# Kernel optimization log

Measured on AMD Instinct MI355X. Metric: run time of the kernel, lower is better.

The kernel has to match this reference:

```python
import jax, jax.numpy as jnp
import numpy as np

B, T, H, DK = 16, 1024, 8, 64  # BN, seq_len, n_heads, d_model/n_heads


def setup_inputs() -> dict:
    key = jax.random.key(0)
    kq, kk, kv = jax.random.split(key, 3)
    queries = jax.random.normal(kq, (B, T, H, DK), dtype=jnp.float32)
    keys = jax.random.normal(kk, (B, T, H, DK), dtype=jnp.float32)
    values = jax.random.normal(kv, (B, T, H, DK), dtype=jnp.float32)
    attention_mask = jnp.zeros((B, H, T, T), dtype=bool)  # mask_flag=False -> unused
    return {"queries": queries, "keys": keys, "values": values,
            "attention_mask": attention_mask}


def reference(queries, keys, values, attention_mask):
    # queries/keys/values: [B, T, H, d]; mask_flag=False so attention_mask unused.
    d_k = queries.shape[-1]
    scale = 1.0 / np.sqrt(d_k).astype(np.float32)
    # scores[b,h,t,s] = sum_e q[b,t,h,e] * k[b,s,h,e]
    scores = jnp.einsum('bthe,bshe->bhts', queries, keys)
    A = jax.nn.softmax(scale * scores, axis=-1)  # dropout=identity (eval)
    V = jnp.einsum('bhts,bshd->bthd', A, values)
    return V
```

## Files before the change

kernel.cpp:

```cpp
#include <hip/hip_runtime.h>
#include <hip/hip_bf16.h>
#include <stdint.h>

typedef __bf16 bf16_t;
typedef bf16_t bf16x8 __attribute__((ext_vector_type(8)));
typedef bf16_t bf16x4 __attribute__((ext_vector_type(4)));
typedef float  f32x4  __attribute__((ext_vector_type(4)));
typedef float  f32x16 __attribute__((ext_vector_type(16)));

constexpr int Bsz = 16, Tsz = 1024, Hn = 8, Dk = 64;
constexpr int QB  = 512;
constexpr int KVB = 64;
constexpr int NIT = Tsz / KVB;
constexpr int STRIDE_T = Hn * Dk;
constexpr float QSCALE = 0.125f * 1.44269504f;

__global__ __launch_bounds__(1024, 4)
void fattn(const float* __restrict__ Q, const float* __restrict__ K,
           const float* __restrict__ V, float* __restrict__ O)
{
    const int orig = blockIdx.x;
    const int wg   = (orig & 7) * 32 + (orig >> 3);
    const int qt   = wg & 1;
    const int bh   = wg >> 1;
    const int h    = bh & (Hn - 1);
    const int b    = bh >> 3;

    const int tid  = threadIdx.x;
    const int warp = tid >> 6;
    const int lane = tid & 63;
    const int l31  = lane & 31;
    const int hi   = lane >> 5;

    __shared__ alignas(16) bf16_t Kl[2][KVB * Dk];
    __shared__ alignas(16) bf16_t Vl[2][Dk * KVB];

    const size_t base = (size_t)b * (Tsz * Hn * Dk) + (size_t)h * Dk;
    const float* Qb = Q + base;
    const float* Kb = K + base;
    const float* Vb = V + base;
    float*       Ob = O + base;

    bf16x8 qf[4];
    {
        const float* qs = Qb + (size_t)(qt * QB + warp * 32 + l31) * STRIDE_T + hi * 8;
        #pragma unroll
        for (int ks = 0; ks < 4; ++ks) {
            f32x4 lo = *reinterpret_cast<const f32x4*>(qs + ks * 16);
            f32x4 hh = *reinterpret_cast<const f32x4*>(qs + ks * 16 + 4);
            bf16x8 f;
            #pragma unroll
            for (int j = 0; j < 4; ++j) {
                f[j]     = (bf16_t)(lo[j] * QSCALE);
                f[4 + j] = (bf16_t)(hh[j] * QSCALE);
            }
            qf[ks] = f;
        }
    }

    const int kr  = tid >> 4;
    const int ke0 = (tid & 15) * 4;
    const float* kg = Kb + (size_t)kr * STRIDE_T + ke0;
    const uint32_t kidx = (uint32_t)(kr * Dk + ke0) ^ (uint32_t)((kr & 7) << 3);

    const int vd   = tid & 63;
    const int pos0 = (tid >> 6) * 4;
    const int vs0  = (pos0 & ~12) | ((pos0 & 4) << 1) | ((pos0 & 8) >> 1);
    const float* vgp = Vb + (size_t)vs0 * STRIDE_T + vd;
    const uint32_t vidx = (uint32_t)(vd * KVB + pos0) ^ (uint32_t)((vd & 7) << 3);

    const uint32_t swz = (uint32_t)((l31 & 7) << 3);

    f32x16 o0, o1;
    #pragma unroll
    for (int r = 0; r < 16; ++r) { o0[r] = 0.f; o1[r] = 0.f; }
    float l_acc = 0.f;

    f32x4 kra;
    float vv[4];
    kra = *reinterpret_cast<const f32x4*>(kg);
    #pragma unroll
    for (int j = 0; j < 4; ++j) vv[j] = vgp[(size_t)j * STRIDE_T];
    {
        bf16x4 kw;
        #pragma unroll
        for (int j = 0; j < 4; ++j) kw[j] = (bf16_t)kra[j];
        *reinterpret_cast<bf16x4*>(&Kl[0][kidx]) = kw;
        bf16x4 vw;
        #pragma unroll
        for (int j = 0; j < 4; ++j) vw[j] = (bf16_t)vv[j];
        *reinterpret_cast<bf16x4*>(&Vl[0][vidx]) = vw;
    }
    __syncthreads();

    for (int t = 0; t < NIT; ++t) {
        const int cur = t & 1;

        if (t + 1 < NIT) {
            kg  += (size_t)KVB * STRIDE_T;
            vgp += (size_t)KVB * STRIDE_T;
            kra = *reinterpret_cast<const f32x4*>(kg);
            #pragma unroll
            for (int j = 0; j < 4; ++j) vv[j] = vgp[(size_t)j * STRIDE_T];
        }


        f32x16 acc0, acc1;
        #pragma unroll
        for (int r = 0; r < 16; ++r) { acc0[r] = 0.f; acc1[r] = 0.f; }
        #pragma unroll
        for (int ks = 0; ks < 4; ++ks) {
            const uint32_t i0 = ((uint32_t)((l31) * Dk + ks * 16 + hi * 8)) ^ swz;
            bf16x8 af0 = *reinterpret_cast<const bf16x8*>(&Kl[cur][i0]);
            acc0 = __builtin_amdgcn_mfma_f32_32x32x16_bf16(af0, qf[ks], acc0, 0, 0, 0);
        }
        #pragma unroll
        for (int ks = 0; ks < 4; ++ks) {
            const uint32_t i1 = ((uint32_t)((32 + l31) * Dk + ks * 16 + hi * 8)) ^ swz;
            bf16x8 af1 = *reinterpret_cast<const bf16x8*>(&Kl[cur][i1]);
            acc1 = __builtin_amdgcn_mfma_f32_32x32x16_bf16(af1, qf[ks], acc1, 0, 0, 0);
        }

        bf16x8 pa00, pa01;
        {
            float p[16];
            #pragma unroll
            for (int r = 0; r < 16; ++r) p[r] = __builtin_exp2f(acc0[r]);
            l_acc += (((p[0]+p[1])+(p[2]+p[3]))+((p[4]+p[5])+(p[6]+p[7])))
                   + (((p[8]+p[9])+(p[10]+p[11]))+((p[12]+p[13])+(p[14]+p[15])));
            #pragma unroll
            for (int j = 0; j < 8; ++j) { pa00[j] = (bf16_t)p[j]; pa01[j] = (bf16_t)p[8+j]; }
        }

        #pragma unroll
        for (int ks2 = 0; ks2 < 2; ++ks2) {
            bf16x8 pa = ks2 ? pa01 : pa00;
            const uint32_t colb = (uint32_t)(ks2 * 16 + hi * 8);
            const uint32_t i0 = ((uint32_t)(l31 * KVB) + colb) ^ swz;
            bf16x8 vf0 = *reinterpret_cast<const bf16x8*>(&Vl[cur][i0]);
            o0 = __builtin_amdgcn_mfma_f32_32x32x16_bf16(vf0, pa, o0, 0, 0, 0);
            const uint32_t i1 = ((uint32_t)((32 + l31) * KVB) + colb) ^ swz;
            bf16x8 vf1 = *reinterpret_cast<const bf16x8*>(&Vl[cur][i1]);
            o1 = __builtin_amdgcn_mfma_f32_32x32x16_bf16(vf1, pa, o1, 0, 0, 0);
        }

        bf16x8 pa10, pa11;
        {
            float p[16];
            #pragma unroll
            for (int r = 0; r < 16; ++r) p[r] = __builtin_exp2f(acc1[r]);
            l_acc += (((p[0]+p[1])+(p[2]+p[3]))+((p[4]+p[5])+(p[6]+p[7])))
                   + (((p[8]+p[9])+(p[10]+p[11]))+((p[12]+p[13])+(p[14]+p[15])));
            #pragma unroll
            for (int j = 0; j < 8; ++j) { pa10[j] = (bf16_t)p[j]; pa11[j] = (bf16_t)p[8+j]; }
        }

        #pragma unroll
        for (int ks2 = 0; ks2 < 2; ++ks2) {
            bf16x8 pa = ks2 ? pa11 : pa10;
            const uint32_t colb = (uint32_t)(32 + ks2 * 16 + hi * 8);
            const uint32_t i0 = ((uint32_t)(l31 * KVB) + colb) ^ swz;
            bf16x8 vf0 = *reinterpret_cast<const bf16x8*>(&Vl[cur][i0]);
            o0 = __builtin_amdgcn_mfma_f32_32x32x16_bf16(vf0, pa, o0, 0, 0, 0);
            const uint32_t i1 = ((uint32_t)((32 + l31) * KVB) + colb) ^ swz;
            bf16x8 vf1 = *reinterpret_cast<const bf16x8*>(&Vl[cur][i1]);
            o1 = __builtin_amdgcn_mfma_f32_32x32x16_bf16(vf1, pa, o1, 0, 0, 0);
        }

        if (t + 1 < NIT) {
            bf16x4 kw;
            #pragma unroll
            for (int j = 0; j < 4; ++j) kw[j] = (bf16_t)kra[j];
            *reinterpret_cast<bf16x4*>(&Kl[cur ^ 1][kidx]) = kw;
            bf16x4 vw;
            #pragma unroll
            for (int j = 0; j < 4; ++j) vw[j] = (bf16_t)vv[j];
            *reinterpret_cast<bf16x4*>(&Vl[cur ^ 1][vidx]) = vw;
        }
        __syncthreads();
    }

    float l_tot = l_acc + __shfl_xor(l_acc, 32, 64);
    const float inv = 1.0f / l_tot;
    float* ob = Ob + (size_t)(qt * QB + warp * 32 + l31) * STRIDE_T;
    #pragma unroll
    for (int r = 0; r < 16; ++r) {
        const int d = (r & 3) + 8 * (r >> 2) + 4 * hi;
        ob[d]      = o0[r] * inv;
        ob[d + 32] = o1[r] * inv;
    }
}

extern "C" void kernel_launch(void* const* d_in, const int* in_sizes, int n_in,
                              void* d_out, int out_size, void* d_ws, size_t ws_size,
                              hipStream_t stream) {
    const float* Q = (const float*)d_in[0];
    const float* K = (const float*)d_in[1];
    const float* V = (const float*)d_in[2];
    float* O = (float*)d_out;

    const int nblocks = Bsz * Hn * (Tsz / QB);
    fattn<<<nblocks, 1024, 0, stream>>>(Q, K, V, O);
}
```

Before: 60.36 us.

## Halve query block to 256 rows with 512-thread blocks and 8-wide staging

```diff
diff --git a/kernel.cpp b/kernel.cpp
--- a/kernel.cpp
+++ b/kernel.cpp
@@ -4,25 +4,24 @@
 
 typedef __bf16 bf16_t;
 typedef bf16_t bf16x8 __attribute__((ext_vector_type(8)));
-typedef bf16_t bf16x4 __attribute__((ext_vector_type(4)));
 typedef float  f32x4  __attribute__((ext_vector_type(4)));
 typedef float  f32x16 __attribute__((ext_vector_type(16)));
 
 constexpr int Bsz = 16, Tsz = 1024, Hn = 8, Dk = 64;
-constexpr int QB  = 512;
+constexpr int QB  = 256;
 constexpr int KVB = 64;
 constexpr int NIT = Tsz / KVB;
 constexpr int STRIDE_T = Hn * Dk;
 constexpr float QSCALE = 0.125f * 1.44269504f;
 
-__global__ __launch_bounds__(1024, 4)
+__global__ __launch_bounds__(512, 4)
 void fattn(const float* __restrict__ Q, const float* __restrict__ K,
            const float* __restrict__ V, float* __restrict__ O)
 {
     const int orig = blockIdx.x;
-    const int wg   = (orig & 7) * 32 + (orig >> 3);
-    const int qt   = wg & 1;
-    const int bh   = wg >> 1;
+    const int wg   = (orig & 7) * 64 + (orig >> 3);
+    const int qt   = wg & 3;
+    const int bh   = wg >> 2;
     const int h    = bh & (Hn - 1);
     const int b    = bh >> 3;
 
@@ -58,14 +57,14 @@
         }
     }
 
-    const int kr  = tid >> 4;
-    const int ke0 = (tid & 15) * 4;
+    const int kr  = tid >> 3;
+    const int ke0 = (tid & 7) * 8;
     const float* kg = Kb + (size_t)kr * STRIDE_T + ke0;
     const uint32_t kidx = (uint32_t)(kr * Dk + ke0) ^ (uint32_t)((kr & 7) << 3);
 
     const int vd   = tid & 63;
-    const int pos0 = (tid >> 6) * 4;
-    const int vs0  = (pos0 & ~12) | ((pos0 & 4) << 1) | ((pos0 & 8) >> 1);
+    const int pos0 = (tid >> 6) * 8;
+    const int vs0  = (pos0 & ~8) | ((pos0 & 8) >> 1);
     const float* vgp = Vb + (size_t)vs0 * STRIDE_T + vd;
     const uint32_t vidx = (uint32_t)(vd * KVB + pos0) ^ (uint32_t)((vd & 7) << 3);
 
@@ -76,20 +75,24 @@
     for (int r = 0; r < 16; ++r) { o0[r] = 0.f; o1[r] = 0.f; }
     float l_acc = 0.f;
 
-    f32x4 kra;
-    float vv[4];
+    f32x4 kra, krb;
+    float vv[8];
     kra = *reinterpret_cast<const f32x4*>(kg);
+    krb = *reinterpret_cast<const f32x4*>(kg + 4);
     #pragma unroll
-    for (int j = 0; j < 4; ++j) vv[j] = vgp[(size_t)j * STRIDE_T];
+    for (int j = 0; j < 8; ++j) {
+        const int off = ((j & 4) << 1) + (j & 3);
+        vv[j] = vgp[(size_t)off * STRIDE_T];
+    }
     {
-        bf16x4 kw;
-        #pragma unroll
-        for (int j = 0; j < 4; ++j) kw[j] = (bf16_t)kra[j];
-        *reinterpret_cast<bf16x4*>(&Kl[0][kidx]) = kw;
-        bf16x4 vw;
-        #pragma unroll
-        for (int j = 0; j < 4; ++j) vw[j] = (bf16_t)vv[j];
-        *reinterpret_cast<bf16x4*>(&Vl[0][vidx]) = vw;
+        bf16x8 kw;
+        #pragma unroll
+        for (int j = 0; j < 4; ++j) { kw[j] = (bf16_t)kra[j]; kw[4 + j] = (bf16_t)krb[j]; }
+        *reinterpret_cast<bf16x8*>(&Kl[0][kidx]) = kw;
+        bf16x8 vw;
+        #pragma unroll
+        for (int j = 0; j < 8; ++j) vw[j] = (bf16_t)vv[j];
+        *reinterpret_cast<bf16x8*>(&Vl[0][vidx]) = vw;
     }
     __syncthreads();
 
@@ -100,10 +103,13 @@
             kg  += (size_t)KVB * STRIDE_T;
             vgp += (size_t)KVB * STRIDE_T;
             kra = *reinterpret_cast<const f32x4*>(kg);
-            #pragma unroll
-            for (int j = 0; j < 4; ++j) vv[j] = vgp[(size_t)j * STRIDE_T];
-        }
-
+            krb = *reinterpret_cast<const f32x4*>(kg + 4);
+            #pragma unroll
+            for (int j = 0; j < 8; ++j) {
+                const int off = ((j & 4) << 1) + (j & 3);
+                vv[j] = vgp[(size_t)off * STRIDE_T];
+            }
+        }
 
         f32x16 acc0, acc1;
         #pragma unroll
@@ -168,14 +174,14 @@
         }
 
         if (t + 1 < NIT) {
-            bf16x4 kw;
-            #pragma unroll
-            for (int j = 0; j < 4; ++j) kw[j] = (bf16_t)kra[j];
-            *reinterpret_cast<bf16x4*>(&Kl[cur ^ 1][kidx]) = kw;
-            bf16x4 vw;
-            #pragma unroll
-            for (int j = 0; j < 4; ++j) vw[j] = (bf16_t)vv[j];
-            *reinterpret_cast<bf16x4*>(&Vl[cur ^ 1][vidx]) = vw;
+            bf16x8 kw;
+            #pragma unroll
+            for (int j = 0; j < 4; ++j) { kw[j] = (bf16_t)kra[j]; kw[4 + j] = (bf16_t)krb[j]; }
+            *reinterpret_cast<bf16x8*>(&Kl[cur ^ 1][kidx]) = kw;
+            bf16x8 vw;
+            #pragma unroll
+            for (int j = 0; j < 8; ++j) vw[j] = (bf16_t)vv[j];
+            *reinterpret_cast<bf16x8*>(&Vl[cur ^ 1][vidx]) = vw;
         }
         __syncthreads();
     }
@@ -200,5 +206,5 @@
     float* O = (float*)d_out;
 
     const int nblocks = Bsz * Hn * (Tsz / QB);
-    fattn<<<nblocks, 1024, 0, stream>>>(Q, K, V, O);
+    fattn<<<nblocks, 512, 0, stream>>>(Q, K, V, O);
 }
```

New measurement: 61.10 us. No clear change (+1.2%).
